# Kernel tuning notes

Measured on AMD Instinct MI355X. Metric: run time of the kernel, lower is better.

Reference implementation:

```python
import jax, jax.numpy as jnp
import numpy as np

N_LAYER, N_HEAD, D_MODEL, D_FF = 6, 16, 1024, 4096
D_HEAD = D_MODEL // N_HEAD            # 64
M_FEAT = 2 * D_MODEL // N_HEAD        # 128, favor_feature_dims default
CHUNK = 128                           # chunk size for causal linear attention
LN_EPS = 1e-5
ATT_EPS = 1e-6                        # fast-transformers CausalLinearAttention eps
B, S = 4, 2048


def _layer_norm(x, g, b):
    mu = x.mean(-1, keepdims=True)
    var = ((x - mu) ** 2).mean(-1, keepdims=True)
    return (x - mu) * jax.lax.rsqrt(var + LN_EPS) * g + b


def _favor_phi(x, omega):
    # x: [B,H,S,Dh]; omega: [Dh, M//2]. FAVOR positive (hyperbolic) random
    # features: phi(x) = [exp(u - |x|^2/2), exp(-u - |x|^2/2)] / sqrt(M),
    # with x pre-scaled by sqrt(softmax_temp), softmax_temp = 1/sqrt(Dh).
    x = x * (D_HEAD ** -0.25)
    u = jnp.einsum('bhsd,dm->bhsm', x, omega)
    nrm = 0.5 * jnp.sum(x * x, axis=-1, keepdims=True)
    phi = jnp.concatenate([jnp.exp(u - nrm), jnp.exp(-u - nrm)], axis=-1)
    return phi * (M_FEAT ** -0.5)


def _causal_linear_attention(Qp, Kp, V):
    # Qp,Kp: [B,H,S,M] nonnegative features; V: [B,H,S,Dh].
    # out_i = phi(q_i)^T S_i / (phi(q_i)^T Z_i + eps),
    # S_i = sum_{j<=i} phi(k_j) v_j^T, Z_i = sum_{j<=i} phi(k_j).
    # Chunked: exclusive chunk prefix sums + masked intra-chunk matmul.
    b, h, s, m = Qp.shape
    d = V.shape[-1]
    c = s // CHUNK
    Qc = Qp.reshape(b, h, c, CHUNK, m)
    Kc = Kp.reshape(b, h, c, CHUNK, m)
    Vc = V.reshape(b, h, c, CHUNK, d)
    kv = jnp.einsum('bhclm,bhcld->bhcmd', Kc, Vc)   # per-chunk K^T V
    ksum = Kc.sum(axis=3)                            # [b,h,c,m]
    kv_pre = jnp.cumsum(kv, axis=2) - kv             # exclusive prefix over chunks
    ks_pre = jnp.cumsum(ksum, axis=2) - ksum
    scores = jnp.einsum('bhcim,bhcjm->bhcij', Qc, Kc)
    mask = jnp.tril(jnp.ones((CHUNK, CHUNK), bool))
    scores = jnp.where(mask, scores, 0.0)            # causal within chunk
    num = (jnp.einsum('bhcij,bhcjd->bhcid', scores, Vc)
           + jnp.einsum('bhcim,bhcmd->bhcid', Qc, kv_pre))
    den = scores.sum(-1) + jnp.einsum('bhcim,bhcm->bhci', Qc, ks_pre)
    out = num / (den[..., None] + ATT_EPS)
    return out.reshape(b, h, s, d)


def _forward(x, Wq, bq, Wk, bk, Wv, bv, Wo, bo, omega,
             g1, be1, W1, bf1, W2, bf2, g2, be2):
    bsz, slen, _ = x.shape
    out = x
    for l in range(N_LAYER):
        def proj(W, bvec):
            y = jnp.einsum('bsd,de->bse', out, W) + bvec
            return y.reshape(bsz, slen, N_HEAD, D_HEAD).transpose(0, 2, 1, 3)
        q = proj(Wq[l], bq[l])
        k = proj(Wk[l], bk[l])
        v = proj(Wv[l], bv[l])
        Qp = _favor_phi(q, omega[l])
        Kp = _favor_phi(k, omega[l])
        a = _causal_linear_attention(Qp, Kp, v)
        a = a.transpose(0, 2, 1, 3).reshape(bsz, slen, D_MODEL)
        a = jnp.einsum('bsd,de->bse', a, Wo[l]) + bo[l]
        h1 = _layer_norm(out + a, g1[l], be1[l])          # post-norm residual 1
        y = jax.nn.relu(jnp.einsum('bsd,df->bsf', h1, W1[l]) + bf1[l])
        y = jnp.einsum('bsf,fd->bsd', y, W2[l]) + bf2[l]
        out = _layer_norm(h1 + y, g2[l], be2[l])          # post-norm residual 2
    return out


def setup_inputs() -> dict:
    key = jax.random.key(0)
    ks = jax.random.split(key, 12)
    s = D_MODEL ** -0.5
    f32 = jnp.float32
    return {
        "x": jax.random.normal(ks[0], (B, S, D_MODEL), f32),
        "Wq": jax.random.normal(ks[1], (N_LAYER, D_MODEL, D_MODEL), f32) * s,
        "bq": jnp.zeros((N_LAYER, D_MODEL), f32),
        "Wk": jax.random.normal(ks[2], (N_LAYER, D_MODEL, D_MODEL), f32) * s,
        "bk": jnp.zeros((N_LAYER, D_MODEL), f32),
        "Wv": jax.random.normal(ks[3], (N_LAYER, D_MODEL, D_MODEL), f32) * s,
        "bv": jnp.zeros((N_LAYER, D_MODEL), f32),
        "Wo": jax.random.normal(ks[4], (N_LAYER, D_MODEL, D_MODEL), f32) * s,
        "bo": jnp.zeros((N_LAYER, D_MODEL), f32),
        "omega": jax.random.normal(ks[5], (N_LAYER, D_HEAD, M_FEAT // 2), f32),
        "g1": jnp.ones((N_LAYER, D_MODEL), f32),
        "be1": jnp.zeros((N_LAYER, D_MODEL), f32),
        "W1": jax.random.normal(ks[6], (N_LAYER, D_MODEL, D_FF), f32) * s,
        "bf1": jnp.zeros((N_LAYER, D_FF), f32),
        "W2": jax.random.normal(ks[7], (N_LAYER, D_FF, D_MODEL), f32) * (D_FF ** -0.5),
        "bf2": jnp.zeros((N_LAYER, D_MODEL), f32),
        "g2": jnp.ones((N_LAYER, D_MODEL), f32),
        "be2": jnp.zeros((N_LAYER, D_MODEL), f32),
    }


def reference(x, Wq, bq, Wk, bk, Wv, bv, Wo, bo, omega,
              g1, be1, W1, bf1, W2, bf2, g2, be2):
    return _forward(x, Wq, bq, Wk, bk, Wv, bv, Wo, bo, omega,
                    g1, be1, W1, bf1, W2, bf2, g2, be2)
```

## Files before the change

### kernel.cpp

```cpp
#include <hip/hip_runtime.h>

typedef unsigned short u16;
typedef __attribute__((ext_vector_type(8))) short bf16x8;
typedef __attribute__((ext_vector_type(4))) float f32x4;

#define DEV __device__ __forceinline__

DEV float b2f(u16 h){ return __uint_as_float(((unsigned)h) << 16); }
DEV u16 f2b(float f){ unsigned u = __float_as_uint(f); u += 0x7FFFu + ((u >> 16) & 1u); return (u16)(u >> 16); }

DEV void gload16(const u16* g, u16* l){
  __builtin_amdgcn_global_load_lds((const __attribute__((address_space(1))) unsigned*)g,
                                   (__attribute__((address_space(3))) unsigned*)l, 16, 0, 0);
}

__global__ __launch_bounds__(256) void wtrans(const float* __restrict__ src, u16* __restrict__ dst,
                                              int K, int N, float scale){
  __shared__ float tile[32][33];
  int k0 = blockIdx.x * 32, n0 = blockIdx.y * 32;
  int tid = threadIdx.x;
#pragma unroll
  for (int i = 0; i < 4; i++){
    int idx = tid + i * 256;
    int r = idx >> 5, c = idx & 31;
    tile[r][c] = src[(size_t)(k0 + r) * N + n0 + c];
  }
  __syncthreads();
#pragma unroll
  for (int i = 0; i < 4; i++){
    int idx = tid + i * 256;
    int r = idx >> 5, c = idx & 31;
    dst[(size_t)(n0 + r) * K + k0 + c] = f2b(tile[c][r] * scale);
  }
}

__global__ __launch_bounds__(256) void cvt16(const float* __restrict__ src, u16* __restrict__ dst){
  size_t i = ((size_t)blockIdx.x * 256 + threadIdx.x) * 4;
  float4 f = *(const float4*)(src + i);
  ushort4 o = make_ushort4(f2b(f.x), f2b(f.y), f2b(f.z), f2b(f.w));
  *(ushort4*)(dst + i) = o;
}

__global__ void catbias(const float* __restrict__ bq, const float* __restrict__ bk,
                        const float* __restrict__ bv, float* __restrict__ bcat){
  int i = blockIdx.x * 256 + threadIdx.x;
  if (i >= 6 * 3072) return;
  int l = i / 3072, j = i % 3072;
  float v = (j < 1024) ? bq[l * 1024 + j] : (j < 2048) ? bk[l * 1024 + j - 1024] : bv[l * 1024 + j - 2048];
  bcat[i] = v;
}

__global__ void fillv(float* __restrict__ p, float v, int n){
  int i = blockIdx.x * 256 + threadIdx.x;
  if (i < n) p[i] = v;
}

DEV int swz(int r){ return (r & 3) ^ ((r >> 2) & 3); }

template<int EPI>
__global__ __launch_bounds__(256) void gemm_bt(const u16* __restrict__ A, const u16* __restrict__ Bt,
                                               const float* __restrict__ bias, void* __restrict__ outp,
                                               int M, int N, int K, int ldA, int ldB){
  __shared__ __align__(16) u16 As[2][4096];
  __shared__ __align__(16) u16 Bs[2][4096];
  const int tid = threadIdx.x;
  const int lane = tid & 63;
  const int w = tid >> 6;
  const int wm = w >> 1, wn = w & 1;
  int nx = gridDim.x;
  int nwg = nx * gridDim.y;
  int lin = blockIdx.y * nx + blockIdx.x;
  int cpx = nwg >> 3;
  int sw = (lin & 7) * cpx + (lin >> 3);
  const int m0 = (sw / nx) * 128;
  const int n0 = (sw % nx) * 128;

  int r0 = tid >> 2, c0 = tid & 3;
  int r1 = r0 + 64;
  int cs0 = c0 ^ swz(r0);
  int cs1 = c0 ^ swz(r1);
  const u16* ag0 = A + (size_t)(m0 + r0) * ldA + cs0 * 8;
  const u16* ag1 = A + (size_t)(m0 + r1) * ldA + cs1 * 8;
  const u16* bg0 = Bt + (size_t)(n0 + r0) * ldB + cs0 * 8;
  const u16* bg1 = Bt + (size_t)(n0 + r1) * ldB + cs1 * 8;

  f32x4 acc[4][4] = {};
  const int KT = K >> 5;

  gload16(ag0, &As[0][w * 512]);
  gload16(ag1, &As[0][2048 + w * 512]);
  gload16(bg0, &Bs[0][w * 512]);
  gload16(bg1, &Bs[0][2048 + w * 512]);

  for (int kt = 0; kt < KT; kt++){
    int cur = kt & 1;
    if (kt + 1 < KT){
      int ko = (kt + 1) << 5;
      gload16(ag0 + ko, &As[cur ^ 1][w * 512]);
      gload16(ag1 + ko, &As[cur ^ 1][2048 + w * 512]);
      gload16(bg0 + ko, &Bs[cur ^ 1][w * 512]);
      gload16(bg1 + ko, &Bs[cur ^ 1][2048 + w * 512]);
      asm volatile("s_waitcnt vmcnt(4)" ::: "memory");
    } else {
      asm volatile("s_waitcnt vmcnt(0)" ::: "memory");
    }
    __builtin_amdgcn_s_barrier();
    bf16x8 fa[4], fb[4];
#pragma unroll
    for (int m = 0; m < 4; m++){
      int row = wm * 64 + m * 16 + (lane & 15);
      int cc = (lane >> 4) ^ swz(row);
      fa[m] = *(const bf16x8*)(&As[cur][row * 32 + cc * 8]);
    }
#pragma unroll
    for (int n = 0; n < 4; n++){
      int row = wn * 64 + n * 16 + (lane & 15);
      int cc = (lane >> 4) ^ swz(row);
      fb[n] = *(const bf16x8*)(&Bs[cur][row * 32 + cc * 8]);
    }
#pragma unroll
    for (int m = 0; m < 4; m++)
#pragma unroll
      for (int n = 0; n < 4; n++)
        acc[m][n] = __builtin_amdgcn_mfma_f32_16x16x32_bf16(fa[m], fb[n], acc[m][n], 0, 0, 0);
    asm volatile("s_waitcnt lgkmcnt(0)" ::: "memory");
    __builtin_amdgcn_s_barrier();
  }

#pragma unroll
  for (int m = 0; m < 4; m++){
    int rowb = m0 + wm * 64 + m * 16 + ((lane >> 4) << 2);
#pragma unroll
    for (int n = 0; n < 4; n++){
      int col = n0 + wn * 64 + n * 16 + (lane & 15);
      float bv = bias[col];
#pragma unroll
      for (int r = 0; r < 4; r++){
        float v = acc[m][n][r] + bv;
        int rr = rowb + r;
        if (EPI == 2) ((u16*)outp)[(size_t)rr * N + col] = f2b(v > 0.f ? v : 0.f);
        else          ((u16*)outp)[(size_t)rr * N + col] = f2b(v);
      }
    }
  }
}

template<int EPI>
__global__ __launch_bounds__(512, 1) void gemm256(const u16* __restrict__ A, const u16* __restrict__ Bt,
                                                  const float* __restrict__ bias, void* __restrict__ outp,
                                                  int M, int N, int K, int ldA, int ldB){
  __shared__ __align__(16) u16 As[3][8192];
  __shared__ __align__(16) u16 Bs[3][8192];
  const int tid = threadIdx.x;
  const int lane = tid & 63;
  const int w = tid >> 6;
  const int wm = w >> 2, wn = w & 3;
  int nx = gridDim.x;
  int nwg = nx * gridDim.y;
  int lin = blockIdx.y * nx + blockIdx.x;
  int cpx = nwg >> 3;
  int sw = (lin & 7) * cpx + (lin >> 3);
  const int m0 = (sw / nx) * 256;
  const int n0 = (sw % nx) * 256;

  int rA0 = tid >> 2, c0 = tid & 3;
  int rA1 = rA0 + 128;
  int csA0 = c0 ^ ((rA0 >> 1) & 3);
  int csA1 = c0 ^ ((rA1 >> 1) & 3);
  const u16* ag0 = A + (size_t)(m0 + rA0) * ldA + csA0 * 8;
  const u16* ag1 = A + (size_t)(m0 + rA1) * ldA + csA1 * 8;
  const u16* bg0 = Bt + (size_t)(n0 + rA0) * ldB + csA0 * 8;
  const u16* bg1 = Bt + (size_t)(n0 + rA1) * ldB + csA1 * 8;

  f32x4 acc[8][4] = {};
  const int KT = K >> 5;

#pragma unroll
  for (int t = 0; t < 2; t++){
    int ko = t << 5;
    gload16(ag0 + ko, &As[t][w * 512]);
    gload16(ag1 + ko, &As[t][4096 + w * 512]);
    gload16(bg0 + ko, &Bs[t][w * 512]);
    gload16(bg1 + ko, &Bs[t][4096 + w * 512]);
  }

  for (int t = 0; t < KT; t++){
    int buf = t % 3;
    if (t + 2 < KT){
      int nb = (t + 2) % 3;
      int ko = (t + 2) << 5;
      gload16(ag0 + ko, &As[nb][w * 512]);
      gload16(ag1 + ko, &As[nb][4096 + w * 512]);
      gload16(bg0 + ko, &Bs[nb][w * 512]);
      gload16(bg1 + ko, &Bs[nb][4096 + w * 512]);
      asm volatile("s_waitcnt vmcnt(8)" ::: "memory");
    } else if (t + 1 < KT){
      asm volatile("s_waitcnt vmcnt(4)" ::: "memory");
    } else {
      asm volatile("s_waitcnt vmcnt(0)" ::: "memory");
    }
    __builtin_amdgcn_s_barrier();
    bf16x8 fa[8], fb[4];
#pragma unroll
    for (int m = 0; m < 8; m++){
      int row = wm * 128 + m * 16 + (lane & 15);
      int cc = (lane >> 4) ^ ((row >> 1) & 3);
      fa[m] = *(const bf16x8*)(&As[buf][row * 32 + cc * 8]);
    }
#pragma unroll
    for (int n = 0; n < 4; n++){
      int row = wn * 64 + n * 16 + (lane & 15);
      int cc = (lane >> 4) ^ ((row >> 1) & 3);
      fb[n] = *(const bf16x8*)(&Bs[buf][row * 32 + cc * 8]);
    }
    __builtin_amdgcn_s_setprio(1);
#pragma unroll
    for (int m = 0; m < 8; m++)
#pragma unroll
      for (int n = 0; n < 4; n++)
        acc[m][n] = __builtin_amdgcn_mfma_f32_16x16x32_bf16(fa[m], fb[n], acc[m][n], 0, 0, 0);
    __builtin_amdgcn_s_setprio(0);
    asm volatile("s_waitcnt lgkmcnt(0)" ::: "memory");
    __builtin_amdgcn_s_barrier();
  }

#pragma unroll
  for (int m = 0; m < 8; m++){
    int rowb = m0 + wm * 128 + m * 16 + ((lane >> 4) << 2);
#pragma unroll
    for (int n = 0; n < 4; n++){
      int col = n0 + wn * 64 + n * 16 + (lane & 15);
      float bv = bias[col];
      if (EPI == 5 && col >= 2048){
        int cv = col - 2048, hh = cv >> 6, dh = cv & 63;
        int bIdx = rowb >> 11, s4 = rowb & 2047;
        ushort4 pk = make_ushort4(f2b(acc[m][n][0] + bv), f2b(acc[m][n][1] + bv),
                                  f2b(acc[m][n][2] + bv), f2b(acc[m][n][3] + bv));
        *(ushort4*)&((u16*)outp + 16777216)[((size_t)(bIdx * 16 + hh) * 64 + dh) * 2048 + s4] = pk;
      } else {
#pragma unroll
        for (int r = 0; r < 4; r++){
          float v = acc[m][n][r] + bv;
          int rr = rowb + r;
          if (EPI == 5){
            u16* dst0 = (u16*)outp + (col < 1024 ? 0 : 8388608);
            int cv = col & 1023, hh = cv >> 6, dh = cv & 63;
            int bIdx = rr >> 11, s = rr & 2047;
            dst0[(((size_t)(bIdx * 16 + hh) * 2048 + s) << 6) + dh] = f2b(v);
          } else {
            ((u16*)outp)[(size_t)rr * N + col] = f2b(v > 0.f ? v : 0.f);
          }
        }
      }
    }
  }
}

__global__ __launch_bounds__(256) void phi2(const u16* __restrict__ qb, const u16* __restrict__ kb,
                                            const u16* __restrict__ omT,
                                            u16* __restrict__ Qp, u16* __restrict__ Kp){
  __shared__ __align__(16) u16 qs[128 * 64];
  __shared__ __align__(16) u16 wl[64 * 64];
  __shared__ __align__(16) u16 ph[128 * 128];
  __shared__ float part[2][128];
  __shared__ float nrm[128];
  int tid = threadIdx.x, w = tid >> 6, lane = tid & 63;
  int blk = blockIdx.x;
  const u16* src; u16* dst; int row0;
  if (blk < 1024){ src = qb; dst = Qp; row0 = blk * 128; }
  else           { src = kb; dst = Kp; row0 = (blk - 1024) * 128; }
  const u16* g = src + (size_t)row0 * 64;
#pragma unroll
  for (int i = 0; i < 4; i++){
    int id = tid * 4 + i;
    int r = id >> 3, kc = id & 7;
    *(bf16x8*)(qs + r * 64 + ((kc ^ (r & 7)) << 3)) = *(const bf16x8*)(g + r * 64 + kc * 8);
  }
#pragma unroll
  for (int i = 0; i < 2; i++){
    int id = tid * 2 + i;
    int m = id >> 3, kc = id & 7;
    *(bf16x8*)(wl + m * 64 + ((kc ^ (m & 7)) << 3)) = *(const bf16x8*)(omT + id * 8);
  }
  __syncthreads();
  {
    int r = tid & 127, half = tid >> 7;
    float s = 0.f;
#pragma unroll
    for (int j = 0; j < 4; j++){
      int kc = half * 4 + j;
      bf16x8 v = *(const bf16x8*)(qs + r * 64 + ((kc ^ (r & 7)) << 3));
#pragma unroll
      for (int e = 0; e < 8; e++){ float f = b2f((u16)v[e]); s += f * f; }
    }
    part[half][r] = s;
  }
  __syncthreads();
  if (tid < 128) nrm[tid] = 0.0625f * (part[0][tid] + part[1][tid]);
  __syncthreads();
  f32x4 acc[2][4] = {};
#pragma unroll
  for (int kt = 0; kt < 2; kt++){
    int kc = kt * 4 + (lane >> 4);
    bf16x8 fa[2], fb[4];
#pragma unroll
    for (int mt = 0; mt < 2; mt++){
      int r = w * 32 + mt * 16 + (lane & 15);
      fa[mt] = *(const bf16x8*)(qs + r * 64 + ((kc ^ (r & 7)) << 3));
    }
#pragma unroll
    for (int nt = 0; nt < 4; nt++){
      int m = nt * 16 + (lane & 15);
      fb[nt] = *(const bf16x8*)(wl + m * 64 + ((kc ^ (m & 7)) << 3));
    }
#pragma unroll
    for (int mt = 0; mt < 2; mt++)
#pragma unroll
      for (int nt = 0; nt < 4; nt++)
        acc[mt][nt] = __builtin_amdgcn_mfma_f32_16x16x32_bf16(fa[mt], fb[nt], acc[mt][nt], 0, 0, 0);
  }
  const float LNC = -2.4260151319598086f;
#pragma unroll
  for (int mt = 0; mt < 2; mt++)
#pragma unroll
    for (int nt = 0; nt < 4; nt++)
#pragma unroll
      for (int r4 = 0; r4 < 4; r4++){
        int r = w * 32 + mt * 16 + ((lane >> 4) << 2) + r4;
        int m = nt * 16 + (lane & 15);
        float u = acc[mt][nt][r4];
        float nr = nrm[r];
        ph[r * 128 + m]      = f2b(__expf(u - nr + LNC));
        ph[r * 128 + 64 + m] = f2b(__expf(-u - nr + LNC));
      }
  __syncthreads();
  u16* go = dst + (size_t)row0 * 128;
#pragma unroll
  for (int i = 0; i < 8; i++){
    int id = i * 256 + tid;
    *(bf16x8*)(go + id * 8) = *(const bf16x8*)(ph + id * 8);
  }
}

__global__ __launch_bounds__(256) void kvchunk(const u16* __restrict__ Kp, const u16* __restrict__ vt,
                                               float* __restrict__ kv, float* __restrict__ ksum){
  __shared__ __align__(16) u16 Ks[128 * 128];
  __shared__ __align__(16) u16 Vst[64 * 128];
  int blk = blockIdx.x; int bh = blk >> 4, c = blk & 15;
  int tid = threadIdx.x;
  size_t base = (size_t)bh * 2048 + c * 128;
  const u16* Kc = Kp + base * 128;
  const u16* vtc = vt + (size_t)bh * 64 * 2048 + c * 128;
  {
    int j = tid >> 1, half = tid & 1;
#pragma unroll
    for (int i = 0; i < 8; i++)
      *(bf16x8*)(Ks + j * 128 + half * 64 + i * 8) = *(const bf16x8*)(Kc + j * 128 + half * 64 + i * 8);
#pragma unroll
    for (int i = 0; i < 4; i++){
      int id = tid * 4 + i;
      int d = id >> 4, mc = id & 15;
      *(bf16x8*)(Vst + d * 128 + mc * 8) = *(const bf16x8*)(vtc + (size_t)d * 2048 + mc * 8);
    }
  }
  __syncthreads();
  int tm = tid & 15, td = tid >> 4;
  int mbase = tm * 8, dbase = td * 4;
  float acc[8][4] = {};
  float ks[8] = {};
  for (int i = 0; i < 128; i++){
    bf16x8 kk = *(const bf16x8*)(Ks + i * 128 + mbase);
    float kf[8];
#pragma unroll
    for (int e = 0; e < 8; e++) kf[e] = b2f((u16)kk[e]);
    float vf[4];
#pragma unroll
    for (int e = 0; e < 4; e++) vf[e] = b2f(Vst[(dbase + e) * 128 + i]);
#pragma unroll
    for (int a = 0; a < 8; a++){
      ks[a] += kf[a];
#pragma unroll
      for (int bb = 0; bb < 4; bb++) acc[a][bb] += kf[a] * vf[bb];
    }
  }
  float* kvout = kv + ((size_t)bh * 16 + c) * 8192;
#pragma unroll
  for (int a = 0; a < 8; a++)
#pragma unroll
    for (int bb = 0; bb < 4; bb++)
      kvout[(size_t)(dbase + bb) * 128 + mbase + a] = acc[a][bb];
  if (td == 0){
    float* kso = ksum + ((size_t)bh * 16 + c) * 128;
#pragma unroll
    for (int a = 0; a < 8; a++) kso[mbase + a] = ks[a];
  }
}

__global__ __launch_bounds__(256) void kvscan(float* __restrict__ kv, float* __restrict__ ksum){
  int bh = blockIdx.x;
  int p = blockIdx.y;
  int tid = threadIdx.x;
  if (p < 8){
    size_t base = (size_t)bh * 16 * 8192;
    int idx0 = p * 1024 + tid;
    for (int rep = 0; rep < 4; rep++){
      int idx = idx0 + rep * 256;
      float run = 0.f;
#pragma unroll
      for (int c = 0; c < 16; c++){
        size_t off = base + (size_t)c * 8192 + idx;
        float v = kv[off]; kv[off] = run; run += v;
      }
    }
  } else if (tid < 128){
    size_t base = (size_t)bh * 16 * 128;
    float run = 0.f;
#pragma unroll
    for (int c = 0; c < 16; c++){
      size_t off = base + c * 128 + tid;
      float v = ksum[off]; ksum[off] = run; run += v;
    }
  }
}

__global__ __launch_bounds__(512) void attn_fused(const u16* __restrict__ Qp, const u16* __restrict__ Kp,
                                                  const u16* __restrict__ vt, const float* __restrict__ kvp,
                                                  const float* __restrict__ ksum, u16* __restrict__ aout){
  __shared__ __align__(16) u16 sm[53248];
  int blk = blockIdx.x, bh = blk >> 4, c = blk & 15;
  int b = bh >> 4, h = bh & 15;
  int tid = threadIdx.x, w = tid >> 6, lane = tid & 63;
  size_t base = (size_t)bh * 2048 + c * 128;
  const u16* Qc = Qp + base * 128;
  const u16* Kc = Kp + base * 128;
  const u16* vtc = vt + (size_t)bh * 64 * 2048 + c * 128;
  const float* kvc = kvp + ((size_t)bh * 16 + c) * 8192;
  const float* ksc = ksum + ((size_t)bh * 16 + c) * 128;
  u16* Qs = sm;
  u16* Ks = sm + 16384;
  u16* B2 = sm + 32768;

#pragma unroll
  for (int i = 0; i < 4; i++){
    int id = tid * 4 + i;
    int r = id >> 4, kc = id & 15;
    int swo = (kc ^ (r & 15)) << 3;
    *(bf16x8*)(Qs + r * 128 + swo) = *(const bf16x8*)(Qc + (size_t)r * 128 + kc * 8);
    *(bf16x8*)(Ks + r * 128 + swo) = *(const bf16x8*)(Kc + (size_t)r * 128 + kc * 8);
  }
#pragma unroll
  for (int i = 0; i < 2; i++){
    int id = tid * 2 + i;
    int d = id >> 4, kc = id & 15;
    *(bf16x8*)(B2 + d * 256 + ((kc ^ (d & 31)) << 3)) = *(const bf16x8*)(vtc + (size_t)d * 2048 + kc * 8);
  }
#pragma unroll
  for (int i = 0; i < 2; i++){
    int id = tid * 2 + i;
    int d = id >> 4, mc = id & 15;
    const float* s8 = kvc + d * 128 + mc * 8;
    float4 f0 = *(const float4*)(s8);
    float4 f1 = *(const float4*)(s8 + 4);
    bf16x8 pk;
    pk[0] = (short)f2b(f0.x); pk[1] = (short)f2b(f0.y); pk[2] = (short)f2b(f0.z); pk[3] = (short)f2b(f0.w);
    pk[4] = (short)f2b(f1.x); pk[5] = (short)f2b(f1.y); pk[6] = (short)f2b(f1.z); pk[7] = (short)f2b(f1.w);
    int kc = 16 + mc;
    *(bf16x8*)(B2 + d * 256 + ((kc ^ (d & 31)) << 3)) = pk;
  }
  {
    int row = 64 + (tid >> 5), kc = tid & 31;
    bf16x8 pk = {};
    if (row == 64){
      if (kc < 16){
#pragma unroll
        for (int e = 0; e < 8; e++) pk[e] = (short)0x3F80;
      } else {
        const float* s8 = ksc + (kc - 16) * 8;
        float4 f0 = *(const float4*)(s8);
        float4 f1 = *(const float4*)(s8 + 4);
        pk[0] = (short)f2b(f0.x); pk[1] = (short)f2b(f0.y); pk[2] = (short)f2b(f0.z); pk[3] = (short)f2b(f0.w);
        pk[4] = (short)f2b(f1.x); pk[5] = (short)f2b(f1.y); pk[6] = (short)f2b(f1.z); pk[7] = (short)f2b(f1.w);
      }
    }
    *(bf16x8*)(B2 + row * 256 + ((kc ^ (row & 31)) << 3)) = pk;
  }
  __syncthreads();

  int wm = w >> 2, wn = w & 3;
  f32x4 acc1[4][2] = {};
#pragma unroll
  for (int kk = 0; kk < 4; kk++){
    int kc = kk * 4 + (lane >> 4);
    bf16x8 fa[4], fb[2];
#pragma unroll
    for (int m = 0; m < 4; m++){
      int row = wm * 64 + m * 16 + (lane & 15);
      fa[m] = *(const bf16x8*)(Qs + row * 128 + ((kc ^ (row & 15)) << 3));
    }
#pragma unroll
    for (int n = 0; n < 2; n++){
      int row = wn * 32 + n * 16 + (lane & 15);
      fb[n] = *(const bf16x8*)(Ks + row * 128 + ((kc ^ (row & 15)) << 3));
    }
#pragma unroll
    for (int m = 0; m < 4; m++)
#pragma unroll
      for (int n = 0; n < 2; n++)
        acc1[m][n] = __builtin_amdgcn_mfma_f32_16x16x32_bf16(fa[m], fb[n], acc1[m][n], 0, 0, 0);
  }
  __syncthreads();

#pragma unroll
  for (int m = 0; m < 4; m++)
#pragma unroll
    for (int n = 0; n < 2; n++)
#pragma unroll
      for (int r = 0; r < 4; r++){
        int i = wm * 64 + m * 16 + ((lane >> 4) << 2) + r;
        int j = wn * 32 + n * 16 + (lane & 15);
        float v = (j <= i) ? acc1[m][n][r] : 0.f;
        Ks[i * 128 + (((j >> 3) ^ (i & 15)) << 3) + (j & 7)] = f2b(v);
      }
  __syncthreads();

  f32x4 acc2[5] = {};
#pragma unroll
  for (int kk = 0; kk < 8; kk++){
    int kc = kk * 4 + (lane >> 4);
    int rowA = w * 16 + (lane & 15);
    bf16x8 fa2;
    if (kk < 4) fa2 = *(const bf16x8*)(Ks + rowA * 128 + ((kc ^ (rowA & 15)) << 3));
    else        fa2 = *(const bf16x8*)(Qs + rowA * 128 + (((kc - 16) ^ (rowA & 15)) << 3));
#pragma unroll
    for (int n = 0; n < 5; n++){
      int d = n * 16 + (lane & 15);
      bf16x8 fb2 = *(const bf16x8*)(B2 + d * 256 + ((kc ^ (d & 31)) << 3));
      acc2[n] = __builtin_amdgcn_mfma_f32_16x16x32_bf16(fa2, fb2, acc2[n], 0, 0, 0);
    }
  }

  float dd[4];
#pragma unroll
  for (int r = 0; r < 4; r++) dd[r] = __shfl(acc2[4][r], lane & 48) + 1e-6f;
  size_t obase = ((size_t)b * 2048 + c * 128) * 1024 + (size_t)h * 64;
#pragma unroll
  for (int n = 0; n < 4; n++)
#pragma unroll
    for (int r = 0; r < 4; r++){
      int i = w * 16 + ((lane >> 4) << 2) + r;
      int d = n * 16 + (lane & 15);
      aout[obase + (size_t)i * 1024 + d] = f2b(acc2[n][r] / dd[r]);
    }
}

__global__ __launch_bounds__(256) void ln_kernel(const float* __restrict__ X1, const u16* __restrict__ X2b,
                                                 const float* __restrict__ g, const float* __restrict__ bb,
                                                 float* __restrict__ outf, u16* __restrict__ outb){
  __shared__ float red[2][4];
  int row = blockIdx.x, tid = threadIdx.x, w = tid >> 6, lane = tid & 63;
  size_t ro = (size_t)row * 1024 + tid * 4;
  float4 a = *(const float4*)(X1 + ro);
  ushort4 bp = *(const ushort4*)(X2b + ro);
  float x0 = a.x + b2f(bp.x), x1 = a.y + b2f(bp.y), x2 = a.z + b2f(bp.z), x3 = a.w + b2f(bp.w);
  float s1 = x0 + x1 + x2 + x3;
  float s2 = x0 * x0 + x1 * x1 + x2 * x2 + x3 * x3;
#pragma unroll
  for (int off = 32; off; off >>= 1){ s1 += __shfl_xor(s1, off); s2 += __shfl_xor(s2, off); }
  if (lane == 0){ red[0][w] = s1; red[1][w] = s2; }
  __syncthreads();
  float t1 = red[0][0] + red[0][1] + red[0][2] + red[0][3];
  float t2 = red[1][0] + red[1][1] + red[1][2] + red[1][3];
  float mu = t1 * (1.f / 1024.f);
  float var = t2 * (1.f / 1024.f) - mu * mu;
  float rs = rsqrtf(var + 1e-5f);
  float4 gv = *(const float4*)(g + tid * 4);
  float4 bv = *(const float4*)(bb + tid * 4);
  float o0 = (x0 - mu) * rs * gv.x + bv.x;
  float o1 = (x1 - mu) * rs * gv.y + bv.y;
  float o2 = (x2 - mu) * rs * gv.z + bv.z;
  float o3 = (x3 - mu) * rs * gv.w + bv.w;
  *(float4*)(outf + ro) = make_float4(o0, o1, o2, o3);
  *(ushort4*)(outb + ro) = make_ushort4(f2b(o0), f2b(o1), f2b(o2), f2b(o3));
}

extern "C" void kernel_launch(void* const* d_in, const int* in_sizes, int n_in,
                              void* d_out, int out_size, void* d_ws, size_t ws_size,
                              hipStream_t stream){
  (void)in_sizes; (void)n_in;
  const float* x   = (const float*)d_in[0];
  const float* Wq  = (const float*)d_in[1];
  const float* bq  = (const float*)d_in[2];
  const float* Wk  = (const float*)d_in[3];
  const float* bk  = (const float*)d_in[4];
  const float* Wv  = (const float*)d_in[5];
  const float* bv  = (const float*)d_in[6];
  const float* Wo  = (const float*)d_in[7];
  const float* bo  = (const float*)d_in[8];
  const float* om  = (const float*)d_in[9];
  const float* g1  = (const float*)d_in[10];
  const float* be1 = (const float*)d_in[11];
  const float* W1  = (const float*)d_in[12];
  const float* bf1 = (const float*)d_in[13];
  const float* W2  = (const float*)d_in[14];
  const float* bf2 = (const float*)d_in[15];
  const float* g2  = (const float*)d_in[16];
  const float* be2 = (const float*)d_in[17];

  char* ws = (char*)d_ws;
  size_t off = 0;
  auto alloc = [&](size_t bytes) -> void* {
    void* p = ws + off; off += (bytes + 255) & ~(size_t)255; return p;
  };
  u16* Wcat = (u16*)alloc(3072ull * 1024 * 2);
  u16* Wot  = (u16*)alloc(1024ull * 1024 * 2);
  u16* W1t  = (u16*)alloc(4096ull * 1024 * 2);
  u16* W2t  = (u16*)alloc(1024ull * 4096 * 2);
  u16* omT  = (u16*)alloc(64ull * 64 * 2);
  float* bcat = (float*)alloc(6ull * 3072 * 4);
  u16* Xb  = (u16*)alloc(8192ull * 1024 * 2);
  u16* qb  = (u16*)alloc(131072ull * 64 * 2);
  u16* kb  = (u16*)alloc(131072ull * 64 * 2);
  u16* vt  = (u16*)alloc(131072ull * 64 * 2);
  u16* Qp  = (u16*)alloc(131072ull * 128 * 2);
  u16* Kp  = (u16*)alloc(131072ull * 128 * 2);
  float* ksum = (float*)alloc(64ull * 16 * 128 * 4);

  if (off > ws_size){
    fillv<<<(out_size + 255) / 256, 256, 0, stream>>>((float*)d_out, (float)(ws_size >> 20), out_size);
    return;
  }

  float* kvbuf  = (float*)qb;
  u16*  ybuf   = qb;
  u16*  wooutb = Qp;
  u16*  w2outb = Qp + 8388608;
  float* h1     = (float*)Kp;
  float* resid  = (float*)d_out;

  cvt16<<<8192, 256, 0, stream>>>(x, Xb);
  catbias<<<72, 256, 0, stream>>>(bq, bk, bv, bcat);

  const float* Xsrc = x;
  for (int l = 0; l < 6; l++){
    size_t o1k = (size_t)l * 1024 * 1024;
    size_t o4k = (size_t)l * 4096 * 1024;
    wtrans<<<dim3(32, 32), 256, 0, stream>>>(Wq + o1k, Wcat, 1024, 1024, 1.f);
    wtrans<<<dim3(32, 32), 256, 0, stream>>>(Wk + o1k, Wcat + 1024ull * 1024, 1024, 1024, 1.f);
    wtrans<<<dim3(32, 32), 256, 0, stream>>>(Wv + o1k, Wcat + 2048ull * 1024, 1024, 1024, 1.f);
    wtrans<<<dim3(32, 32), 256, 0, stream>>>(Wo + o1k, Wot, 1024, 1024, 1.f);
    wtrans<<<dim3(32, 128), 256, 0, stream>>>(W1 + o4k, W1t, 1024, 4096, 1.f);
    wtrans<<<dim3(128, 32), 256, 0, stream>>>(W2 + o4k, W2t, 4096, 1024, 1.f);
    wtrans<<<dim3(2, 2), 256, 0, stream>>>(om + (size_t)l * 4096, omT, 64, 64, 0.35355339059327373f);

    gemm256<5><<<dim3(12, 32), 512, 0, stream>>>(Xb, Wcat, bcat + l * 3072, qb, 8192, 3072, 1024, 1024, 1024);
    phi2<<<2048, 256, 0, stream>>>(qb, kb, omT, Qp, Kp);
    kvchunk<<<1024, 256, 0, stream>>>(Kp, vt, kvbuf, ksum);
    kvscan<<<dim3(64, 9), 256, 0, stream>>>(kvbuf, ksum);
    attn_fused<<<1024, 512, 0, stream>>>(Qp, Kp, vt, kvbuf, ksum, Xb);
    gemm_bt<6><<<dim3(8, 64), 256, 0, stream>>>(Xb, Wot, bo + l * 1024, wooutb, 8192, 1024, 1024, 1024, 1024);
    ln_kernel<<<8192, 256, 0, stream>>>(Xsrc, wooutb, g1 + l * 1024, be1 + l * 1024, h1, Xb);
    gemm256<2><<<dim3(16, 32), 512, 0, stream>>>(Xb, W1t, bf1 + l * 4096, ybuf, 8192, 4096, 1024, 1024, 1024);
    gemm_bt<6><<<dim3(8, 64), 256, 0, stream>>>(ybuf, W2t, bf2 + l * 1024, w2outb, 8192, 1024, 4096, 4096, 4096);
    ln_kernel<<<8192, 256, 0, stream>>>(h1, w2outb, g2 + l * 1024, be2 + l * 1024, resid, Xb);
    Xsrc = resid;
  }
}
```

Before: 2.756 ms.

## Replace 256-tile GEMM with K=64 double-buffered interleaved-prefetch GEMM; move QKV to gemm_bt

The 256x256 GEMM used for the FFN up-projection is rewritten to use a 64-wide K step with two LDS buffers. Next-tile loads for A and B are interleaved between the two halves of each sub-step's MFMA work, instead of a three-stage ring of 32-wide K tiles. The aim is fewer barriers per K and better overlap of global-to-LDS loads with MFMAs. The QKV projection is moved to the smaller 128-tile gemm_bt kernel, which gains the head-split and transposed-V epilogue; this changes tile size and occupancy for that GEMM.

```diff
diff --git a/kernel.cpp b/kernel.cpp
--- a/kernel.cpp
+++ b/kernel.cpp
@@ -134,23 +134,39 @@
     for (int n = 0; n < 4; n++){
       int col = n0 + wn * 64 + n * 16 + (lane & 15);
       float bv = bias[col];
-#pragma unroll
-      for (int r = 0; r < 4; r++){
-        float v = acc[m][n][r] + bv;
-        int rr = rowb + r;
-        if (EPI == 2) ((u16*)outp)[(size_t)rr * N + col] = f2b(v > 0.f ? v : 0.f);
-        else          ((u16*)outp)[(size_t)rr * N + col] = f2b(v);
+      if (EPI == 5 && col >= 2048){
+        int cv = col - 2048, hh = cv >> 6, dh = cv & 63;
+        int bIdx = rowb >> 11, s4 = rowb & 2047;
+        ushort4 pk = make_ushort4(f2b(acc[m][n][0] + bv), f2b(acc[m][n][1] + bv),
+                                  f2b(acc[m][n][2] + bv), f2b(acc[m][n][3] + bv));
+        *(ushort4*)&((u16*)outp + 16777216)[((size_t)(bIdx * 16 + hh) * 64 + dh) * 2048 + s4] = pk;
+      } else {
+#pragma unroll
+        for (int r = 0; r < 4; r++){
+          float v = acc[m][n][r] + bv;
+          int rr = rowb + r;
+          if (EPI == 5){
+            u16* dst0 = (u16*)outp + (col < 1024 ? 0 : 8388608);
+            int cv = col & 1023, hh = cv >> 6, dh = cv & 63;
+            int bIdx = rr >> 11, s = rr & 2047;
+            dst0[(((size_t)(bIdx * 16 + hh) * 2048 + s) << 6) + dh] = f2b(v);
+          } else if (EPI == 2){
+            ((u16*)outp)[(size_t)rr * N + col] = f2b(v > 0.f ? v : 0.f);
+          } else {
+            ((u16*)outp)[(size_t)rr * N + col] = f2b(v);
+          }
+        }
       }
     }
   }
 }
 
 template<int EPI>
-__global__ __launch_bounds__(512, 1) void gemm256(const u16* __restrict__ A, const u16* __restrict__ Bt,
-                                                  const float* __restrict__ bias, void* __restrict__ outp,
-                                                  int M, int N, int K, int ldA, int ldB){
-  __shared__ __align__(16) u16 As[3][8192];
-  __shared__ __align__(16) u16 Bs[3][8192];
+__global__ __launch_bounds__(512, 1) void gemm8p(const u16* __restrict__ A, const u16* __restrict__ Bt,
+                                                 const float* __restrict__ bias, void* __restrict__ outp,
+                                                 int M, int N, int K, int ldA, int ldB){
+  __shared__ __align__(16) u16 As[2][16384];
+  __shared__ __align__(16) u16 Bs[2][16384];
   const int tid = threadIdx.x;
   const int lane = tid & 63;
   const int w = tid >> 6;
@@ -163,65 +179,82 @@
   const int m0 = (sw / nx) * 256;
   const int n0 = (sw % nx) * 256;
 
-  int rA0 = tid >> 2, c0 = tid & 3;
-  int rA1 = rA0 + 128;
-  int csA0 = c0 ^ ((rA0 >> 1) & 3);
-  int csA1 = c0 ^ ((rA1 >> 1) & 3);
-  const u16* ag0 = A + (size_t)(m0 + rA0) * ldA + csA0 * 8;
-  const u16* ag1 = A + (size_t)(m0 + rA1) * ldA + csA1 * 8;
-  const u16* bg0 = Bt + (size_t)(n0 + rA0) * ldB + csA0 * 8;
-  const u16* bg1 = Bt + (size_t)(n0 + rA1) * ldB + csA1 * 8;
+  const int id0 = tid;
+  const int id1 = 512 + tid;
+  const int r0 = id0 >> 2, c20 = id0 & 3;
+  const int r1 = id1 >> 2, c21 = id1 & 3;
+  const int cs0 = c20 ^ ((r0 >> 1) & 3);
+  const int cs1 = c21 ^ ((r1 >> 1) & 3);
+  const u16* Ag0 = A + (size_t)(m0 + r0) * ldA + cs0 * 8;
+  const u16* Ag1 = A + (size_t)(m0 + r1) * ldA + cs1 * 8;
+  const u16* Bg0 = Bt + (size_t)(n0 + r0) * ldB + cs0 * 8;
+  const u16* Bg1 = Bt + (size_t)(n0 + r1) * ldB + cs1 * 8;
 
   f32x4 acc[8][4] = {};
-  const int KT = K >> 5;
-
-#pragma unroll
-  for (int t = 0; t < 2; t++){
-    int ko = t << 5;
-    gload16(ag0 + ko, &As[t][w * 512]);
-    gload16(ag1 + ko, &As[t][4096 + w * 512]);
-    gload16(bg0 + ko, &Bs[t][w * 512]);
-    gload16(bg1 + ko, &Bs[t][4096 + w * 512]);
-  }
+  const int KT = K >> 6;
+
+  auto stA = [&](int buf, int kt, int ks){
+    int kc = kt * 64 + ks * 32;
+    gload16(Ag0 + kc, &As[buf][ks * 8192 + w * 512]);
+    gload16(Ag1 + kc, &As[buf][ks * 8192 + 4096 + w * 512]);
+  };
+  auto stB = [&](int buf, int kt, int ks){
+    int kc = kt * 64 + ks * 32;
+    gload16(Bg0 + kc, &Bs[buf][ks * 8192 + w * 512]);
+    gload16(Bg1 + kc, &Bs[buf][ks * 8192 + 4096 + w * 512]);
+  };
+
+  stA(0, 0, 0); stB(0, 0, 0); stA(0, 0, 1); stB(0, 0, 1);
 
   for (int t = 0; t < KT; t++){
-    int buf = t % 3;
-    if (t + 2 < KT){
-      int nb = (t + 2) % 3;
-      int ko = (t + 2) << 5;
-      gload16(ag0 + ko, &As[nb][w * 512]);
-      gload16(ag1 + ko, &As[nb][4096 + w * 512]);
-      gload16(bg0 + ko, &Bs[nb][w * 512]);
-      gload16(bg1 + ko, &Bs[nb][4096 + w * 512]);
-      asm volatile("s_waitcnt vmcnt(8)" ::: "memory");
-    } else if (t + 1 < KT){
-      asm volatile("s_waitcnt vmcnt(4)" ::: "memory");
-    } else {
-      asm volatile("s_waitcnt vmcnt(0)" ::: "memory");
-    }
+    int c = t & 1, nb = c ^ 1;
+    bool pf = (t + 1 < KT);
+    asm volatile("s_waitcnt vmcnt(4)" ::: "memory");
     __builtin_amdgcn_s_barrier();
-    bf16x8 fa[8], fb[4];
-#pragma unroll
-    for (int m = 0; m < 8; m++){
-      int row = wm * 128 + m * 16 + (lane & 15);
-      int cc = (lane >> 4) ^ ((row >> 1) & 3);
-      fa[m] = *(const bf16x8*)(&As[buf][row * 32 + cc * 8]);
-    }
-#pragma unroll
-    for (int n = 0; n < 4; n++){
-      int row = wn * 64 + n * 16 + (lane & 15);
-      int cc = (lane >> 4) ^ ((row >> 1) & 3);
-      fb[n] = *(const bf16x8*)(&Bs[buf][row * 32 + cc * 8]);
-    }
-    __builtin_amdgcn_s_setprio(1);
-#pragma unroll
-    for (int m = 0; m < 8; m++)
-#pragma unroll
-      for (int n = 0; n < 4; n++)
-        acc[m][n] = __builtin_amdgcn_mfma_f32_16x16x32_bf16(fa[m], fb[n], acc[m][n], 0, 0, 0);
-    __builtin_amdgcn_s_setprio(0);
-    asm volatile("s_waitcnt lgkmcnt(0)" ::: "memory");
-    __builtin_amdgcn_s_barrier();
+
+#pragma unroll
+    for (int ks = 0; ks < 2; ks++){
+      if (ks == 1){
+        if (pf) asm volatile("s_waitcnt vmcnt(4)" ::: "memory");
+        else    asm volatile("s_waitcnt vmcnt(0)" ::: "memory");
+        __builtin_amdgcn_s_barrier();
+      }
+      if (pf){ if (ks == 0) stA(nb, t + 1, 0); else stA(nb, t + 1, 1); }
+      bf16x8 fa[8], fb[2];
+#pragma unroll
+      for (int m = 0; m < 8; m++){
+        int row = wm * 128 + m * 16 + (lane & 15);
+        int slot = (lane >> 4) ^ ((row >> 1) & 3);
+        fa[m] = *(const bf16x8*)(&As[c][ks * 8192 + row * 32 + slot * 8]);
+      }
+#pragma unroll
+      for (int nn = 0; nn < 2; nn++){
+        int row = wn * 64 + nn * 16 + (lane & 15);
+        int slot = (lane >> 4) ^ ((row >> 1) & 3);
+        fb[nn] = *(const bf16x8*)(&Bs[c][ks * 8192 + row * 32 + slot * 8]);
+      }
+      __builtin_amdgcn_s_setprio(1);
+#pragma unroll
+      for (int m = 0; m < 8; m++)
+#pragma unroll
+        for (int nn = 0; nn < 2; nn++)
+          acc[m][nn] = __builtin_amdgcn_mfma_f32_16x16x32_bf16(fa[m], fb[nn], acc[m][nn], 0, 0, 0);
+      __builtin_amdgcn_s_setprio(0);
+      if (pf){ if (ks == 0) stB(nb, t + 1, 0); else stB(nb, t + 1, 1); }
+#pragma unroll
+      for (int nn = 0; nn < 2; nn++){
+        int row = wn * 64 + 32 + nn * 16 + (lane & 15);
+        int slot = (lane >> 4) ^ ((row >> 1) & 3);
+        fb[nn] = *(const bf16x8*)(&Bs[c][ks * 8192 + row * 32 + slot * 8]);
+      }
+      __builtin_amdgcn_s_setprio(1);
+#pragma unroll
+      for (int m = 0; m < 8; m++)
+#pragma unroll
+        for (int nn = 0; nn < 2; nn++)
+          acc[m][2 + nn] = __builtin_amdgcn_mfma_f32_16x16x32_bf16(fa[m], fb[nn], acc[m][2 + nn], 0, 0, 0);
+      __builtin_amdgcn_s_setprio(0);
+    }
   }
 
 #pragma unroll
@@ -231,26 +264,11 @@
     for (int n = 0; n < 4; n++){
       int col = n0 + wn * 64 + n * 16 + (lane & 15);
       float bv = bias[col];
-      if (EPI == 5 && col >= 2048){
-        int cv = col - 2048, hh = cv >> 6, dh = cv & 63;
-        int bIdx = rowb >> 11, s4 = rowb & 2047;
-        ushort4 pk = make_ushort4(f2b(acc[m][n][0] + bv), f2b(acc[m][n][1] + bv),
-                                  f2b(acc[m][n][2] + bv), f2b(acc[m][n][3] + bv));
-        *(ushort4*)&((u16*)outp + 16777216)[((size_t)(bIdx * 16 + hh) * 64 + dh) * 2048 + s4] = pk;
-      } else {
-#pragma unroll
-        for (int r = 0; r < 4; r++){
-          float v = acc[m][n][r] + bv;
-          int rr = rowb + r;
-          if (EPI == 5){
-            u16* dst0 = (u16*)outp + (col < 1024 ? 0 : 8388608);
-            int cv = col & 1023, hh = cv >> 6, dh = cv & 63;
-            int bIdx = rr >> 11, s = rr & 2047;
-            dst0[(((size_t)(bIdx * 16 + hh) * 2048 + s) << 6) + dh] = f2b(v);
-          } else {
-            ((u16*)outp)[(size_t)rr * N + col] = f2b(v > 0.f ? v : 0.f);
-          }
-        }
+#pragma unroll
+      for (int r = 0; r < 4; r++){
+        float v = acc[m][n][r] + bv;
+        int rr = rowb + r;
+        ((u16*)outp)[(size_t)rr * N + col] = f2b(v > 0.f ? v : 0.f);
       }
     }
   }
@@ -652,14 +670,14 @@
     wtrans<<<dim3(128, 32), 256, 0, stream>>>(W2 + o4k, W2t, 4096, 1024, 1.f);
     wtrans<<<dim3(2, 2), 256, 0, stream>>>(om + (size_t)l * 4096, omT, 64, 64, 0.35355339059327373f);
 
-    gemm256<5><<<dim3(12, 32), 512, 0, stream>>>(Xb, Wcat, bcat + l * 3072, qb, 8192, 3072, 1024, 1024, 1024);
+    gemm_bt<5><<<dim3(24, 64), 256, 0, stream>>>(Xb, Wcat, bcat + l * 3072, qb, 8192, 3072, 1024, 1024, 1024);
     phi2<<<2048, 256, 0, stream>>>(qb, kb, omT, Qp, Kp);
     kvchunk<<<1024, 256, 0, stream>>>(Kp, vt, kvbuf, ksum);
     kvscan<<<dim3(64, 9), 256, 0, stream>>>(kvbuf, ksum);
     attn_fused<<<1024, 512, 0, stream>>>(Qp, Kp, vt, kvbuf, ksum, Xb);
     gemm_bt<6><<<dim3(8, 64), 256, 0, stream>>>(Xb, Wot, bo + l * 1024, wooutb, 8192, 1024, 1024, 1024, 1024);
     ln_kernel<<<8192, 256, 0, stream>>>(Xsrc, wooutb, g1 + l * 1024, be1 + l * 1024, h1, Xb);
-    gemm256<2><<<dim3(16, 32), 512, 0, stream>>>(Xb, W1t, bf1 + l * 4096, ybuf, 8192, 4096, 1024, 1024, 1024);
+    gemm8p<2><<<dim3(16, 32), 512, 0, stream>>>(Xb, W1t, bf1 + l * 4096, ybuf, 8192, 4096, 1024, 1024, 1024);
     gemm_bt<6><<<dim3(8, 64), 256, 0, stream>>>(ybuf, W2t, bf2 + l * 1024, w2outb, 8192, 1024, 4096, 4096, 4096);
     ln_kernel<<<8192, 256, 0, stream>>>(h1, w2outb, g2 + l * 1024, be2 + l * 1024, resid, Xb);
     Xsrc = resid;
```

New measurement: 2.630 ms. -4.6%, faster.
